# Kernel tuning notes

Measured on AMD Instinct MI355X. Metric: run time of the kernel, lower is better.

The kernel has to match this reference:

```python
import jax, jax.numpy as jnp
import numpy as np


def _mhc_kernels():
    # Malvar-He-Cutler 5x5 interpolation kernels, shape (4, 1, 5, 5) OIHW
    G_at_RB = np.array([[0, 0, -1, 0, 0], [0, 0, 2, 0, 0], [-1, 2, 4, 2, -1],
                        [0, 0, 2, 0, 0], [0, 0, -1, 0, 0]], dtype=np.float32) / 8
    R_at_G_Rrow = np.array([[0, 0, 0.5, 0, 0], [0, -1, 0, -1, 0], [-1, 4, 5, 4, -1],
                            [0, -1, 0, -1, 0], [0, 0, 0.5, 0, 0]], dtype=np.float32) / 8
    R_at_G_Brow = np.array([[0, 0, -1, 0, 0], [0, -1, 4, -1, 0], [0.5, 0, 5, 0, 0.5],
                            [0, -1, 4, -1, 0], [0, 0, -1, 0, 0]], dtype=np.float32) / 8
    R_at_B = np.array([[0, 0, -1.5, 0, 0], [0, 2, 0, 2, 0], [-1.5, 0, 6, 0, -1.5],
                       [0, 2, 0, 2, 0], [0, 0, -1.5, 0, 0]], dtype=np.float32) / 8
    return np.stack([G_at_RB, R_at_G_Rrow, R_at_G_Brow, R_at_B], axis=0)[:, None, :, :]


def setup_inputs() -> dict:
    key = jax.random.key(0)
    H, W = 4096, 6144  # 24 MP raw frame
    x = jax.random.randint(key, (H, W), 0, 16777216, dtype=jnp.int32)
    kernels = jnp.asarray(_mhc_kernels())  # fixed buffer values, (4,1,5,5)
    return {"x": x, "kernels": kernels}


def reference(x, kernels):
    xf = x.astype(jnp.float32)  # [H, W]
    # reflect pad by 2 and convolve with the 4 MHC kernels in one conv
    xp = jnp.pad(xf, 2, mode="reflect")[None, None]  # [1,1,H+4,W+4]
    res = jax.lax.conv_general_dilated(
        xp, kernels, window_strides=(1, 1), padding="VALID",
        dimension_numbers=("NCHW", "OIHW", "NCHW"))[0]  # [4, H, W]
    Gi, Rgr, Rgb, Rb = res[0], res[1], res[2], res[3]

    z = jnp.zeros_like(xf)
    # RGGB mosaic: R at (even,even), G at (even,odd)+(odd,even), B at (odd,odd)
    R = (z.at[::2, ::2].set(xf[::2, ::2])
           .at[::2, 1::2].set(Rgr[::2, 1::2])
           .at[1::2, ::2].set(Rgb[1::2, ::2])
           .at[1::2, 1::2].set(Rb[1::2, 1::2]))
    G = (z.at[::2, 1::2].set(xf[::2, 1::2])
           .at[1::2, ::2].set(xf[1::2, ::2])
           .at[::2, ::2].set(Gi[::2, ::2])
           .at[1::2, 1::2].set(Gi[1::2, 1::2]))
    B = (z.at[1::2, 1::2].set(xf[1::2, 1::2])
           .at[1::2, ::2].set(Rgr[1::2, ::2])
           .at[::2, 1::2].set(Rgb[::2, 1::2])
           .at[::2, ::2].set(Rb[::2, ::2]))

    rgb = jnp.stack([R, G, B], axis=-1)  # [H, W, 3]
    return jnp.clip(rgb, 0, 16777215).astype(jnp.int32)
```

## Files before the change

kernel.cpp:

```cpp
#include <hip/hip_runtime.h>

#define IMG_H 4096
#define IMG_W 6144

constexpr int SH  = 32;
constexpr int NSX = IMG_W / 128;
constexpr int NSY = IMG_H / SH;

typedef int i2 __attribute__((ext_vector_type(2)));

__device__ __forceinline__ int reflect_h(int r) {
    return r < 0 ? -r : (r >= IMG_H ? 2 * IMG_H - 2 - r : r);
}
__device__ __forceinline__ int clampi(float v) {
    return (int)fminf(fmaxf(v, 0.f), 16777215.f);
}

struct Row { i2 a, b, c; int fix; };

__global__ __launch_bounds__(256)
void demosaic(const int* __restrict__ x, int* __restrict__ out) {
    const int wid  = blockIdx.x * 4 + (threadIdx.x >> 6);
    const int lane = threadIdx.x & 63;
    const int sx = wid >> 7;
    const int sy = wid & (NSY - 1);
    const int gx0 = sx * 128;
    const int gy0 = sy * SH;
    const int ce  = gx0 + 2 * lane;

    const int  cA = max(ce - 2, 0);
    const int  cB = ce;
    const int  cC = min(ce + 2, IMG_W - 2);
    const bool pL = (ce == 0), pR = (ce == IMG_W - 2);
    const bool pat = pL || pR;
    const int  fixc = pL ? 2 : IMG_W - 3;

    auto issue = [&](int y, Row& R) {
        const int* rp = x + (long)reflect_h(y) * IMG_W;
        R.a = *(const i2*)(rp + cA);
        R.b = *(const i2*)(rp + cB);
        R.c = *(const i2*)(rp + cC);
        if (pat) R.fix = rp[fixc];
    };
    auto consume = [&](const Row& R, float* w6) {
        w6[0] = (float)R.a.x; w6[1] = (float)R.a.y;
        w6[2] = (float)R.b.x; w6[3] = (float)R.b.y;
        w6[4] = (float)R.c.x; w6[5] = (float)R.c.y;
        if (pat) { float f = (float)R.fix; if (pL) w6[0] = f; else w6[5] = f; }
    };

    float w[5][6];
    {
        Row t[4];
        #pragma unroll
        for (int i = 0; i < 4; ++i) issue(gy0 - 2 + i, t[i]);
        #pragma unroll
        for (int i = 0; i < 4; ++i) consume(t[i], w[i]);
    }
    Row pr[2];
    issue(gy0 + 2, pr[0]);
    issue(gy0 + 3, pr[1]);

    int* op = out + (long)gy0 * (IMG_W * 3) + ce * 3;

    for (int i = 0; i < SH; i += 2) {
        consume(pr[0], w[4]);
        if (i < SH - 2) issue(gy0 + i + 4, pr[0]);
        {
            float Ge = (-w[0][2] + 2.f*(w[1][2]+w[3][2]) + 4.f*w[2][2] - w[4][2]
                        - w[2][0] + 2.f*(w[2][1]+w[2][3]) - w[2][4]) * 0.125f;
            float Ce = (-1.5f*(w[0][2]+w[4][2]+w[2][0]+w[2][4])
                        + 2.f*(w[1][1]+w[1][3]+w[3][1]+w[3][3]) + 6.f*w[2][2]) * 0.125f;
            float RRo = (0.5f*(w[0][3]+w[4][3]) - (w[1][2]+w[1][4]+w[3][2]+w[3][4])
                         - (w[2][1]+w[2][5]) + 4.f*(w[2][2]+w[2][4]) + 5.f*w[2][3]) * 0.125f;
            float RBo = (-(w[0][3]+w[4][3]) - (w[1][2]+w[1][4]+w[3][2]+w[3][4])
                         + 4.f*(w[1][3]+w[3][3]) + 0.5f*(w[2][1]+w[2][5]) + 5.f*w[2][3]) * 0.125f;
            i2 q0, q1, q2;
            q0.x = clampi(w[2][2]); q0.y = clampi(Ge);
            q1.x = clampi(Ce);      q1.y = clampi(RRo);
            q2.x = clampi(w[2][3]); q2.y = clampi(RBo);
            __builtin_nontemporal_store(q0, (i2*)op);
            __builtin_nontemporal_store(q1, (i2*)(op + 2));
            __builtin_nontemporal_store(q2, (i2*)(op + 4));
        }
        #pragma unroll
        for (int r = 0; r < 4; ++r)
            #pragma unroll
            for (int c = 0; c < 6; ++c) w[r][c] = w[r+1][c];
        op += IMG_W * 3;

        consume(pr[1], w[4]);
        if (i < SH - 3) issue(gy0 + i + 5, pr[1]);
        {
            float RBe = (-(w[0][2]+w[4][2]) - (w[1][1]+w[1][3]+w[3][1]+w[3][3])
                         + 4.f*(w[1][2]+w[3][2]) + 0.5f*(w[2][0]+w[2][4]) + 5.f*w[2][2]) * 0.125f;
            float RRe = (0.5f*(w[0][2]+w[4][2]) - (w[1][1]+w[1][3]+w[3][1]+w[3][3])
                         - (w[2][0]+w[2][4]) + 4.f*(w[2][1]+w[2][3]) + 5.f*w[2][2]) * 0.125f;
            float Co  = (-1.5f*(w[0][3]+w[4][3]+w[2][1]+w[2][5])
                         + 2.f*(w[1][2]+w[1][4]+w[3][2]+w[3][4]) + 6.f*w[2][3]) * 0.125f;
            float Go  = (-w[0][3] + 2.f*(w[1][3]+w[3][3]) + 4.f*w[2][3] - w[4][3]
                         - w[2][1] + 2.f*(w[2][2]+w[2][4]) - w[2][5]) * 0.125f;
            i2 q0, q1, q2;
            q0.x = clampi(RBe);     q0.y = clampi(w[2][2]);
            q1.x = clampi(RRe);     q1.y = clampi(Co);
            q2.x = clampi(Go);      q2.y = clampi(w[2][3]);
            __builtin_nontemporal_store(q0, (i2*)op);
            __builtin_nontemporal_store(q1, (i2*)(op + 2));
            __builtin_nontemporal_store(q2, (i2*)(op + 4));
        }
        #pragma unroll
        for (int r = 0; r < 4; ++r)
            #pragma unroll
            for (int c = 0; c < 6; ++c) w[r][c] = w[r+1][c];
        op += IMG_W * 3;
    }
}

extern "C" void kernel_launch(void* const* d_in, const int* in_sizes, int n_in,
                              void* d_out, int out_size, void* d_ws, size_t ws_size,
                              hipStream_t stream) {
    const int* x = (const int*)d_in[0];
    int* out = (int*)d_out;
    demosaic<<<NSX * NSY / 4, 256, 0, stream>>>(x, out);
}
```

Before: 393.7 us.

## Stage output rows through LDS for 16-byte coalesced stores and deepen prefetch

```diff
diff --git a/kernel.cpp b/kernel.cpp
--- a/kernel.cpp
+++ b/kernel.cpp
@@ -6,8 +6,10 @@
 constexpr int SH  = 32;
 constexpr int NSX = IMG_W / 128;
 constexpr int NSY = IMG_H / SH;
+constexpr int RS  = IMG_W * 3;
 
 typedef int i2 __attribute__((ext_vector_type(2)));
+typedef int i4 __attribute__((ext_vector_type(4)));
 
 __device__ __forceinline__ int reflect_h(int r) {
     return r < 0 ? -r : (r >= IMG_H ? 2 * IMG_H - 2 - r : r);
@@ -20,8 +22,13 @@
 
 __global__ __launch_bounds__(256)
 void demosaic(const int* __restrict__ x, int* __restrict__ out) {
-    const int wid  = blockIdx.x * 4 + (threadIdx.x >> 6);
-    const int lane = threadIdx.x & 63;
+    __shared__ __align__(16) int sbuf[4][2][768];
+
+    const int tid  = threadIdx.x;
+    const int wv   = tid >> 6;
+    const int wid  = blockIdx.x * 4 + wv;
+    const int lane = tid & 63;
+
     const int sx = wid >> 7;
     const int sy = wid & (NSY - 1);
     const int gx0 = sx * 128;
@@ -49,23 +56,33 @@
         if (pat) { float f = (float)R.fix; if (pL) w6[0] = f; else w6[5] = f; }
     };
 
-    float w[5][6];
+    int doff[3];
+    #pragma unroll
+    for (int c = 0; c < 3; ++c) {
+        int off = c * 256 + 4 * lane;
+        doff[c] = (off >= 384) ? (off - 384 + RS) : off;
+    }
+
+    float w[6][6];
     {
-        Row t[4];
-        #pragma unroll
-        for (int i = 0; i < 4; ++i) issue(gy0 - 2 + i, t[i]);
-        #pragma unroll
-        for (int i = 0; i < 4; ++i) consume(t[i], w[i]);
+        Row t0, t1, t2, t3;
+        issue(gy0 - 2, t0); issue(gy0 - 1, t1);
+        issue(gy0 + 0, t2); issue(gy0 + 1, t3);
+        consume(t0, w[0]); consume(t1, w[1]);
+        consume(t2, w[2]); consume(t3, w[3]);
     }
-    Row pr[2];
-    issue(gy0 + 2, pr[0]);
-    issue(gy0 + 3, pr[1]);
+    Row pr0, pr1, pr2, pr3;
+    issue(gy0 + 2, pr0); issue(gy0 + 3, pr1);
+    issue(gy0 + 4, pr2); issue(gy0 + 5, pr3);
 
-    int* op = out + (long)gy0 * (IMG_W * 3) + ce * 3;
+    int* op = out + (long)gy0 * RS + gx0 * 3;
 
-    for (int i = 0; i < SH; i += 2) {
-        consume(pr[0], w[4]);
-        if (i < SH - 2) issue(gy0 + i + 4, pr[0]);
+    auto body = [&](int i, Row& A, Row& B, int* sb) {
+        consume(A, w[4]);
+        consume(B, w[5]);
+        if (i + 6 <= SH + 1) issue(gy0 + i + 6, A);
+        if (i + 7 <= SH + 1) issue(gy0 + i + 7, B);
+
         {
             float Ge = (-w[0][2] + 2.f*(w[1][2]+w[3][2]) + 4.f*w[2][2] - w[4][2]
                         - w[2][0] + 2.f*(w[2][1]+w[2][3]) - w[2][4]) * 0.125f;
@@ -75,44 +92,50 @@
                          - (w[2][1]+w[2][5]) + 4.f*(w[2][2]+w[2][4]) + 5.f*w[2][3]) * 0.125f;
             float RBo = (-(w[0][3]+w[4][3]) - (w[1][2]+w[1][4]+w[3][2]+w[3][4])
                          + 4.f*(w[1][3]+w[3][3]) + 0.5f*(w[2][1]+w[2][5]) + 5.f*w[2][3]) * 0.125f;
-            i2 q0, q1, q2;
-            q0.x = clampi(w[2][2]); q0.y = clampi(Ge);
-            q1.x = clampi(Ce);      q1.y = clampi(RRo);
-            q2.x = clampi(w[2][3]); q2.y = clampi(RBo);
-            __builtin_nontemporal_store(q0, (i2*)op);
-            __builtin_nontemporal_store(q1, (i2*)(op + 2));
-            __builtin_nontemporal_store(q2, (i2*)(op + 4));
+            i2 q;
+            q.x = clampi(w[2][2]); q.y = clampi(Ge);  *(i2*)&sb[6*lane + 0] = q;
+            q.x = clampi(Ce);      q.y = clampi(RRo); *(i2*)&sb[6*lane + 2] = q;
+            q.x = clampi(w[2][3]); q.y = clampi(RBo); *(i2*)&sb[6*lane + 4] = q;
         }
+        {
+            float RBe = (-(w[1][2]+w[5][2]) - (w[2][1]+w[2][3]+w[4][1]+w[4][3])
+                         + 4.f*(w[2][2]+w[4][2]) + 0.5f*(w[3][0]+w[3][4]) + 5.f*w[3][2]) * 0.125f;
+            float RRe = (0.5f*(w[1][2]+w[5][2]) - (w[2][1]+w[2][3]+w[4][1]+w[4][3])
+                         - (w[3][0]+w[3][4]) + 4.f*(w[3][1]+w[3][3]) + 5.f*w[3][2]) * 0.125f;
+            float Co  = (-1.5f*(w[1][3]+w[5][3]+w[3][1]+w[3][5])
+                         + 2.f*(w[2][2]+w[2][4]+w[4][2]+w[4][4]) + 6.f*w[3][3]) * 0.125f;
+            float Go  = (-w[1][3] + 2.f*(w[2][3]+w[4][3]) + 4.f*w[3][3] - w[5][3]
+                         - w[3][1] + 2.f*(w[3][2]+w[3][4]) - w[3][5]) * 0.125f;
+            i2 q;
+            q.x = clampi(RBe);     q.y = clampi(w[3][2]); *(i2*)&sb[384 + 6*lane + 0] = q;
+            q.x = clampi(RRe);     q.y = clampi(Co);      *(i2*)&sb[384 + 6*lane + 2] = q;
+            q.x = clampi(Go);      q.y = clampi(w[3][3]); *(i2*)&sb[384 + 6*lane + 4] = q;
+        }
+
+        asm volatile("s_waitcnt lgkmcnt(0)" ::: "memory");
+        __builtin_amdgcn_sched_barrier(0);
+
+        #pragma unroll
+        for (int c = 0; c < 3; ++c) {
+            i2 lo = *(const i2*)&sb[c * 256 + 4 * lane];
+            i2 hi = *(const i2*)&sb[c * 256 + 4 * lane + 2];
+            i4 q; q.x = lo.x; q.y = lo.y; q.z = hi.x; q.w = hi.y;
+            __builtin_nontemporal_store(q, (i4*)(op + doff[c]));
+        }
+        asm volatile("" ::: "memory");
+        op += 2 * RS;
+
         #pragma unroll
         for (int r = 0; r < 4; ++r)
             #pragma unroll
-            for (int c = 0; c < 6; ++c) w[r][c] = w[r+1][c];
-        op += IMG_W * 3;
+            for (int c6 = 0; c6 < 6; ++c6) w[r][c6] = w[r + 2][c6];
+    };
 
-        consume(pr[1], w[4]);
-        if (i < SH - 3) issue(gy0 + i + 5, pr[1]);
-        {
-            float RBe = (-(w[0][2]+w[4][2]) - (w[1][1]+w[1][3]+w[3][1]+w[3][3])
-                         + 4.f*(w[1][2]+w[3][2]) + 0.5f*(w[2][0]+w[2][4]) + 5.f*w[2][2]) * 0.125f;
-            float RRe = (0.5f*(w[0][2]+w[4][2]) - (w[1][1]+w[1][3]+w[3][1]+w[3][3])
-                         - (w[2][0]+w[2][4]) + 4.f*(w[2][1]+w[2][3]) + 5.f*w[2][2]) * 0.125f;
-            float Co  = (-1.5f*(w[0][3]+w[4][3]+w[2][1]+w[2][5])
-                         + 2.f*(w[1][2]+w[1][4]+w[3][2]+w[3][4]) + 6.f*w[2][3]) * 0.125f;
-            float Go  = (-w[0][3] + 2.f*(w[1][3]+w[3][3]) + 4.f*w[2][3] - w[4][3]
-                         - w[2][1] + 2.f*(w[2][2]+w[2][4]) - w[2][5]) * 0.125f;
-            i2 q0, q1, q2;
-            q0.x = clampi(RBe);     q0.y = clampi(w[2][2]);
-            q1.x = clampi(RRe);     q1.y = clampi(Co);
-            q2.x = clampi(Go);      q2.y = clampi(w[2][3]);
-            __builtin_nontemporal_store(q0, (i2*)op);
-            __builtin_nontemporal_store(q1, (i2*)(op + 2));
-            __builtin_nontemporal_store(q2, (i2*)(op + 4));
-        }
-        #pragma unroll
-        for (int r = 0; r < 4; ++r)
-            #pragma unroll
-            for (int c = 0; c < 6; ++c) w[r][c] = w[r+1][c];
-        op += IMG_W * 3;
+    int* sb0 = sbuf[wv][0];
+    int* sb1 = sbuf[wv][1];
+    for (int i = 0; i < SH; i += 4) {
+        body(i,     pr0, pr1, sb0);
+        body(i + 2, pr2, pr3, sb1);
     }
 }
 
```

Measured after the change: 380.2 us. 3.4% less time.
